# Optimization experiments

Hardware: AMD Instinct MI355X
Metric: run time of the kernel (lower is better)

## Reference

```python
import jax, jax.numpy as jnp
import numpy as np

N_NODES = 50000
N_EDGES = 600000
DIN, DH, DOUT = 128, 256, 128
BN_EPS = 1e-5
LRELU_SLOPE = 0.01


def setup_inputs() -> dict:
    key = jax.random.key(0)
    ks = jax.random.split(key, 16)
    rn = lambda k, s, sc=0.05: jax.random.normal(k, s, dtype=jnp.float32) * sc
    return {
        'nodes': jax.random.normal(ks[0], (N_NODES, DIN), dtype=jnp.float32),
        'src': jax.random.randint(ks[1], (N_EDGES,), 0, N_NODES, dtype=jnp.int32),
        'dst': jax.random.randint(ks[2], (N_EDGES,), 0, N_NODES, dtype=jnp.int32),
        # FeedForward params
        'Wf1': rn(ks[3], (DIN, DH)), 'bf1': jnp.zeros((DH,), jnp.float32),
        'gf1': jnp.ones((DH,), jnp.float32), 'bef1': jnp.zeros((DH,), jnp.float32),
        'Wf2': rn(ks[4], (DH, DIN)), 'bf2': jnp.zeros((DIN,), jnp.float32),
        'gf2': jnp.ones((DIN,), jnp.float32), 'bef2': jnp.zeros((DIN,), jnp.float32),
        # SAGEConv 1 (in->hidden)
        'Ws1': rn(ks[5], (DIN, DH)), 'Wn1': rn(ks[6], (DIN, DH)), 'b1': jnp.zeros((DH,), jnp.float32),
        'gs1': jnp.ones((DH,), jnp.float32), 'bs1': jnp.zeros((DH,), jnp.float32),
        # SAGEConv 2 (hidden->out)
        'Ws2': rn(ks[7], (DH, DOUT)), 'Wn2': rn(ks[8], (DH, DOUT)), 'b2': jnp.zeros((DOUT,), jnp.float32),
        'gs2': jnp.ones((DOUT,), jnp.float32), 'bs2': jnp.zeros((DOUT,), jnp.float32),
    }


def _bn(x, gamma, beta):
    # BatchNorm1d, training mode: batch stats over node dim, biased variance
    mu = jnp.mean(x, axis=0)
    var = jnp.mean(jnp.square(x - mu), axis=0)
    return (x - mu) * jax.lax.rsqrt(var + BN_EPS) * gamma + beta


def _sage_mean(x, src, dst, Wself, Wneigh, bias):
    # DGL SAGEConv('mean'): out = x@Wself + mean_{src->dst}(x[src])@Wneigh + bias
    n = x.shape[0]
    deg = jax.ops.segment_sum(jnp.ones_like(src, dtype=x.dtype), dst, num_segments=n)
    agg = jax.ops.segment_sum(x[src], dst, num_segments=n)  # [N, d] irregular scatter-add
    h_neigh = agg / jnp.maximum(deg, 1.0)[:, None]
    return x @ Wself + h_neigh @ Wneigh + bias


def reference(nodes, src, dst, Wf1, bf1, gf1, bef1, Wf2, bf2, gf2, bef2,
              Ws1, Wn1, b1, gs1, bs1, Ws2, Wn2, b2, gs2, bs2):
    # FeedForward (dropout=0 -> identity)
    h = jax.nn.relu(_bn(nodes @ Wf1 + bf1, gf1, bef1))
    h = jax.nn.relu(_bn(h @ Wf2 + bf2, gf2, bef2))
    # SAGE layer 1
    h1 = _sage_mean(h, src, dst, Ws1, Wn1, b1)
    h1 = jax.nn.leaky_relu(_bn(h1, gs1, bs1), LRELU_SLOPE)
    # SAGE layer 2
    h2 = _sage_mean(h1, src, dst, Ws2, Wn2, b2)
    return jax.nn.leaky_relu(_bn(h2, gs2, bs2), LRELU_SLOPE)
```

## Files before the change

kernel.cpp:

```cpp
#include <hip/hip_runtime.h>

#define DIN 128
#define BN_EPS 1e-5f

typedef __attribute__((ext_vector_type(8))) short bf16x8;
typedef __attribute__((ext_vector_type(8))) unsigned short us8;
typedef __attribute__((ext_vector_type(4))) float f32x4;

__device__ __forceinline__ ushort f2bf(float f) {
    unsigned u = __float_as_uint(f);
    u += 0x7fffu + ((u >> 16) & 1u);
    return (ushort)(u >> 16);
}
__device__ __forceinline__ float bf2f(ushort h) {
    return __uint_as_float(((unsigned)h) << 16);
}

template<int KC, int STATS>
__global__ __launch_bounds__(256) void gemm_wreg(
    const ushort* __restrict__ A, const ushort* __restrict__ BT,
    ushort* __restrict__ C, int mStrips, int N, int K, int logNG,
    float* __restrict__ gsums, float* __restrict__ gsqs)
{
    int tid = threadIdx.x;
    int lane = tid & 63;
    int gw = blockIdx.x * 4 + (tid >> 6);
    int wg = gw & ((1 << logNG) - 1);
    int set = gw >> logNG;
    int totalSets = (gridDim.x * 4) >> logNG;
    int cl = lane & 15, q = lane >> 4;
    int colBase = wg * 64;

    bf16x8 bf[4][KC];
    #pragma unroll
    for (int nt = 0; nt < 4; nt++) {
        const ushort* bp = BT + (long)(colBase + nt * 16 + cl) * K + q * 8;
        #pragma unroll
        for (int kc = 0; kc < KC; kc++)
            bf[nt][kc] = *(const bf16x8*)(bp + kc * 32);
    }

    float ssum[4] = {0.f, 0.f, 0.f, 0.f};
    float ssq[4]  = {0.f, 0.f, 0.f, 0.f};

    for (int strip = set; strip < mStrips; strip += totalSets) {
        int rowBase = strip * 16;
        const ushort* ap = A + (long)(rowBase + cl) * K + q * 8;
        bf16x8 af[KC];
        #pragma unroll
        for (int kc = 0; kc < KC; kc++)
            af[kc] = *(const bf16x8*)(ap + kc * 32);
        f32x4 acc[4] = {};
        #pragma unroll
        for (int kc = 0; kc < KC; kc++)
            #pragma unroll
            for (int nt = 0; nt < 4; nt++)
                acc[nt] = __builtin_amdgcn_mfma_f32_16x16x32_bf16(af[kc], bf[nt][kc], acc[nt], 0, 0, 0);
        #pragma unroll
        for (int nt = 0; nt < 4; nt++) {
            #pragma unroll
            for (int r = 0; r < 4; r++) {
                float v = acc[nt][r];
                long row = rowBase + q * 4 + r;
                C[row * N + colBase + nt * 16 + cl] = f2bf(v);
                if (STATS) { ssum[nt] += v; ssq[nt] += v * v; }
            }
        }
    }

    if (STATS) {
        #pragma unroll
        for (int nt = 0; nt < 4; nt++) {
            ssum[nt] += __shfl_xor(ssum[nt], 16, 64);
            ssum[nt] += __shfl_xor(ssum[nt], 32, 64);
            ssq[nt]  += __shfl_xor(ssq[nt], 16, 64);
            ssq[nt]  += __shfl_xor(ssq[nt], 32, 64);
        }
        if (q == 0) {
            #pragma unroll
            for (int nt = 0; nt < 4; nt++) {
                atomicAdd(&gsums[colBase + nt * 16 + cl], ssum[nt]);
                atomicAdd(&gsqs[colBase + nt * 16 + cl], ssq[nt]);
            }
        }
    }
}

__global__ __launch_bounds__(256) void setup_all(
    const float* __restrict__ nodes, ushort* __restrict__ Xbf, int nConv4, int nbConv,
    const float* __restrict__ W0, const float* __restrict__ W1,
    const float* __restrict__ W2, const float* __restrict__ W3,
    const float* __restrict__ W4, const float* __restrict__ W5,
    ushort* __restrict__ WT,
    int* __restrict__ zeroInts, int nZero4, int nbZero,
    float* __restrict__ stats)
{
    int b = blockIdx.x;
    int tid = threadIdx.x;
    if (b < nbConv) {
        int t = b * 256 + tid;
        if (t < nConv4) {
            float4 v = *(const float4*)&nodes[(long)t * 4];
            ushort4 o; o.x = f2bf(v.x); o.y = f2bf(v.y); o.z = f2bf(v.z); o.w = f2bf(v.w);
            *(ushort4*)&Xbf[(long)t * 4] = o;
        }
        return;
    }
    b -= nbConv;
    if (b < 768) {
        int seg = b >> 7;
        const float* W; int logK, dstBase, stride, kOff;
        switch (seg) {
            case 0: W = W0; logK = 7; dstBase = 0;      stride = 128; kOff = 0;   break;
            case 1: W = W1; logK = 8; dstBase = 32768;  stride = 256; kOff = 0;   break;
            case 2: W = W2; logK = 7; dstBase = 65536;  stride = 256; kOff = 0;   break;
            case 3: W = W3; logK = 7; dstBase = 65536;  stride = 256; kOff = 128; break;
            case 4: W = W4; logK = 8; dstBase = 131072; stride = 256; kOff = 0;   break;
            default:W = W5; logK = 8; dstBase = 163840; stride = 256; kOff = 0;   break;
        }
        int t = (b & 127) * 256 + tid;
        int N = 32768 >> logK;
        int k = t & ((1 << logK) - 1);
        int n = t >> logK;
        WT[(long)dstBase + (long)n * stride + kOff + k] = f2bf(W[(long)k * N + n]);
        return;
    }
    b -= 768;
    if (b < nbZero) {
        int t = b * 256 + tid;
        if (t < nZero4) *(int4*)&zeroInts[(long)t * 4] = make_int4(0, 0, 0, 0);
        return;
    }
    b -= nbZero;
    int t = b * 256 + tid;
    if (t < 512) *(float4*)&stats[(long)t * 4] = make_float4(0, 0, 0, 0);
}

template<int LOGN>
__global__ __launch_bounds__(256) void bnact_bf16(
    const ushort* __restrict__ X,
    const float* __restrict__ sums, const float* __restrict__ sqs,
    const float* __restrict__ gamma, const float* __restrict__ beta, float invM,
    ushort* __restrict__ O, int nRows, int outStride, float negSlope)
{
    constexpr int NCH = 1 << LOGN;
    __shared__ float ssc[NCH], ssh[NCH];
    int tid = threadIdx.x;
    if (tid < NCH) {
        float mean = sums[tid] * invM;
        float var = sqs[tid] * invM - mean * mean;
        float sc = gamma[tid] * rsqrtf(var + BN_EPS);
        ssc[tid] = sc;
        ssh[tid] = beta[tid] - mean * sc;
    }
    __syncthreads();
    int cb = (tid * 8) & (NCH - 1);
    float4 sA = *(const float4*)&ssc[cb];
    float4 sB = *(const float4*)&ssc[cb + 4];
    float4 hA = *(const float4*)&ssh[cb];
    float4 hB = *(const float4*)&ssh[cb + 4];
    const int rpb = (256 * 8) >> LOGN;
    int r0 = blockIdx.x * rpb + ((tid * 8) >> LOGN);
    int rstride = gridDim.x * rpb;
    for (int row = r0; row < nRows; row += rstride) {
        us8 v = *(const us8*)&X[(long)row * NCH + cb];
        float f0 = bf2f(v[0]) * sA.x + hA.x; f0 = (f0 > 0.f) ? f0 : f0 * negSlope;
        float f1 = bf2f(v[1]) * sA.y + hA.y; f1 = (f1 > 0.f) ? f1 : f1 * negSlope;
        float f2 = bf2f(v[2]) * sA.z + hA.z; f2 = (f2 > 0.f) ? f2 : f2 * negSlope;
        float f3 = bf2f(v[3]) * sA.w + hA.w; f3 = (f3 > 0.f) ? f3 : f3 * negSlope;
        float f4 = bf2f(v[4]) * sB.x + hB.x; f4 = (f4 > 0.f) ? f4 : f4 * negSlope;
        float f5 = bf2f(v[5]) * sB.y + hB.y; f5 = (f5 > 0.f) ? f5 : f5 * negSlope;
        float f6 = bf2f(v[6]) * sB.z + hB.z; f6 = (f6 > 0.f) ? f6 : f6 * negSlope;
        float f7 = bf2f(v[7]) * sB.w + hB.w; f7 = (f7 > 0.f) ? f7 : f7 * negSlope;
        us8 o;
        o[0] = f2bf(f0); o[1] = f2bf(f1); o[2] = f2bf(f2); o[3] = f2bf(f3);
        o[4] = f2bf(f4); o[5] = f2bf(f5); o[6] = f2bf(f6); o[7] = f2bf(f7);
        *(us8*)&O[(long)row * outStride + cb] = o;
    }
}

__global__ __launch_bounds__(256) void bnact_f32(
    float* __restrict__ X,
    const float* __restrict__ sums, const float* __restrict__ sqs,
    const float* __restrict__ gamma, const float* __restrict__ beta, float invM,
    int nRows, float negSlope)
{
    __shared__ float ssc[128], ssh[128];
    int tid = threadIdx.x;
    if (tid < 128) {
        float mean = sums[tid] * invM;
        float var = sqs[tid] * invM - mean * mean;
        float sc = gamma[tid] * rsqrtf(var + BN_EPS);
        ssc[tid] = sc;
        ssh[tid] = beta[tid] - mean * sc;
    }
    __syncthreads();
    int cb = (tid * 4) & 127;
    float4 sc = *(const float4*)&ssc[cb];
    float4 sh = *(const float4*)&ssh[cb];
    int r0 = blockIdx.x * 8 + ((tid * 4) >> 7);
    int rstride = gridDim.x * 8;
    for (int row = r0; row < nRows; row += rstride) {
        float4 v = *(const float4*)&X[(long)row * 128 + cb];
        float a = v.x * sc.x + sh.x; a = (a > 0.f) ? a : a * negSlope;
        float b = v.y * sc.y + sh.y; b = (b > 0.f) ? b : b * negSlope;
        float d = v.z * sc.z + sh.z; d = (d > 0.f) ? d : d * negSlope;
        float e = v.w * sc.w + sh.w; e = (e > 0.f) ? e : e * negSlope;
        *(float4*)&X[(long)row * 128 + cb] = make_float4(a, b, d, e);
    }
}

__global__ __launch_bounds__(256) void colstats128(
    const float* __restrict__ X, float* __restrict__ sums, float* __restrict__ sqs, int M)
{
    __shared__ float ss[128], sq[128];
    int tid = threadIdx.x;
    if (tid < 128) { ss[tid] = 0.f; sq[tid] = 0.f; }
    __syncthreads();
    int cg = tid & 31;
    int worker = (blockIdx.x << 3) | (tid >> 5);
    int totalW = gridDim.x << 3;
    float4 s4 = make_float4(0, 0, 0, 0), q4 = make_float4(0, 0, 0, 0);
    for (int r = worker; r < M; r += totalW) {
        float4 v = *(const float4*)&X[(long)r * 128 + cg * 4];
        s4.x += v.x; s4.y += v.y; s4.z += v.z; s4.w += v.w;
        q4.x += v.x * v.x; q4.y += v.y * v.y; q4.z += v.z * v.z; q4.w += v.w * v.w;
    }
    atomicAdd(&ss[cg * 4 + 0], s4.x); atomicAdd(&sq[cg * 4 + 0], q4.x);
    atomicAdd(&ss[cg * 4 + 1], s4.y); atomicAdd(&sq[cg * 4 + 1], q4.y);
    atomicAdd(&ss[cg * 4 + 2], s4.z); atomicAdd(&sq[cg * 4 + 2], q4.z);
    atomicAdd(&ss[cg * 4 + 3], s4.w); atomicAdd(&sq[cg * 4 + 3], q4.w);
    __syncthreads();
    if (tid < 128) { atomicAdd(&sums[tid], ss[tid]); atomicAdd(&sqs[tid], sq[tid]); }
}

__global__ void degcount_kernel(const int* __restrict__ dst, int* __restrict__ degi, int E)
{
    int i = blockIdx.x * blockDim.x + threadIdx.x;
    if (i < E) atomicAdd(&degi[dst[i]], 1);
}

__global__ __launch_bounds__(256) void scan_block_sums(const int* __restrict__ degi,
                                                       int* __restrict__ partial, int n)
{
    __shared__ int s[256];
    int i = blockIdx.x * 256 + threadIdx.x;
    s[threadIdx.x] = (i < n) ? degi[i] : 0;
    __syncthreads();
    for (int off = 128; off > 0; off >>= 1) {
        if (threadIdx.x < off) s[threadIdx.x] += s[threadIdx.x + off];
        __syncthreads();
    }
    if (threadIdx.x == 0) partial[blockIdx.x] = s[0];
}

__global__ __launch_bounds__(256) void scan_final(const int* __restrict__ degi,
                                                  const int* __restrict__ partial,
                                                  int* __restrict__ rowstart, int n, int nb)
{
    __shared__ int s[256];
    __shared__ int ps[256];
    int tid = threadIdx.x;
    ps[tid] = (tid < nb && tid < (int)blockIdx.x) ? partial[tid] : 0;
    __syncthreads();
    for (int off = 128; off > 0; off >>= 1) {
        if (tid < off) ps[tid] += ps[tid + off];
        __syncthreads();
    }
    int offset = ps[0];
    int i = blockIdx.x * 256 + tid;
    int v = (i < n) ? degi[i] : 0;
    s[tid] = v;
    __syncthreads();
    for (int off = 1; off < 256; off <<= 1) {
        int t = (tid >= off) ? s[tid - off] : 0;
        __syncthreads();
        s[tid] += t;
        __syncthreads();
    }
    if (i < n) rowstart[i] = offset + s[tid] - v;
}

__global__ void fillcsr_kernel(const int* __restrict__ src, const int* __restrict__ dst,
                               const int* __restrict__ rowstart, int* __restrict__ cursor,
                               int* __restrict__ csr, int E)
{
    int i = blockIdx.x * blockDim.x + threadIdx.x;
    if (i < E) {
        int d = dst[i];
        int p = atomicAdd(&cursor[d], 1);
        csr[rowstart[d] + p] = src[i];
    }
}

__device__ __forceinline__ void acc8(float acc[8], us8 v) {
    #pragma unroll
    for (int e = 0; e < 8; e++) acc[e] += bf2f(v[e]);
}

__global__ __launch_bounds__(256) void gather16_bf(
    const ushort* __restrict__ X, const int* __restrict__ rowstart,
    const int* __restrict__ degi, const int* __restrict__ csr,
    ushort* __restrict__ O, int nN)
{
    int wv = (blockIdx.x * blockDim.x + threadIdx.x) >> 6;
    int lane = threadIdx.x & 63;
    if (wv >= nN) return;
    int g = lane >> 4;
    int sc = lane & 15;
    int start = rowstart[wv], d = degi[wv];
    const ushort* Xc = X + sc * 8;
    float acc[8] = {};
    if (d > 0) {
        int dm = (d < 64) ? d : 64;
        int idx_l = csr[start + ((lane < dm) ? lane : (dm - 1))];
        int j = 0;
        for (; j + 8 <= dm; j += 8) {
            int i0 = __shfl(idx_l, j + g, 64);
            int i1 = __shfl(idx_l, j + 4 + g, 64);
            us8 v0 = *(const us8*)(Xc + (long)i0 * 256);
            us8 v1 = *(const us8*)(Xc + (long)i1 * 256);
            acc8(acc, v0);
            acc8(acc, v1);
        }
        if (j + 4 <= dm) {
            int i0 = __shfl(idx_l, j + g, 64);
            us8 v0 = *(const us8*)(Xc + (long)i0 * 256);
            acc8(acc, v0);
            j += 4;
        }
        int rem = dm - j;
        if (rem > 0) {
            int sl = j + ((g < rem) ? g : (rem - 1));
            int i0 = __shfl(idx_l, sl, 64);
            if (g < rem) {
                us8 v0 = *(const us8*)(Xc + (long)i0 * 256);
                acc8(acc, v0);
            }
        }
        for (int jj = 64; jj < d; jj += 4) {
            if (jj + g < d) {
                int i0 = csr[start + jj + g];
                us8 v0 = *(const us8*)(Xc + (long)i0 * 256);
                acc8(acc, v0);
            }
        }
    }
    #pragma unroll
    for (int e = 0; e < 8; e++) {
        acc[e] += __shfl_xor(acc[e], 16, 64);
        acc[e] += __shfl_xor(acc[e], 32, 64);
    }
    if (g == 0) {
        float inv = 1.f / fmaxf((float)d, 1.f);
        us8 o;
        #pragma unroll
        for (int e = 0; e < 8; e++) o[e] = f2bf(acc[e] * inv);
        *(us8*)(O + (long)wv * 256 + sc * 8) = o;
    }
}

__global__ __launch_bounds__(256) void gather16_fuse(
    const ushort* __restrict__ Z, const int* __restrict__ rowstart,
    const int* __restrict__ degi, const int* __restrict__ csr,
    float* __restrict__ O, int nN)
{
    int wv = (blockIdx.x * blockDim.x + threadIdx.x) >> 6;
    int lane = threadIdx.x & 63;
    if (wv >= nN) return;
    int g = lane >> 4;
    int sc = lane & 15;
    int start = rowstart[wv], d = degi[wv];
    const ushort* Zc = Z + sc * 8;
    us8 selfv = *(const us8*)(Zc + (long)wv * 256 + 128);
    float acc[8] = {};
    if (d > 0) {
        int dm = (d < 64) ? d : 64;
        int idx_l = csr[start + ((lane < dm) ? lane : (dm - 1))];
        int j = 0;
        for (; j + 8 <= dm; j += 8) {
            int i0 = __shfl(idx_l, j + g, 64);
            int i1 = __shfl(idx_l, j + 4 + g, 64);
            us8 v0 = *(const us8*)(Zc + (long)i0 * 256);
            us8 v1 = *(const us8*)(Zc + (long)i1 * 256);
            acc8(acc, v0);
            acc8(acc, v1);
        }
        if (j + 4 <= dm) {
            int i0 = __shfl(idx_l, j + g, 64);
            us8 v0 = *(const us8*)(Zc + (long)i0 * 256);
            acc8(acc, v0);
            j += 4;
        }
        int rem = dm - j;
        if (rem > 0) {
            int sl = j + ((g < rem) ? g : (rem - 1));
            int i0 = __shfl(idx_l, sl, 64);
            if (g < rem) {
                us8 v0 = *(const us8*)(Zc + (long)i0 * 256);
                acc8(acc, v0);
            }
        }
        for (int jj = 64; jj < d; jj += 4) {
            if (jj + g < d) {
                int i0 = csr[start + jj + g];
                us8 v0 = *(const us8*)(Zc + (long)i0 * 256);
                acc8(acc, v0);
            }
        }
    }
    #pragma unroll
    for (int e = 0; e < 8; e++) {
        acc[e] += __shfl_xor(acc[e], 16, 64);
        acc[e] += __shfl_xor(acc[e], 32, 64);
    }
    if (g == 0) {
        float inv = 1.f / fmaxf((float)d, 1.f);
        float r[8];
        #pragma unroll
        for (int e = 0; e < 8; e++) r[e] = acc[e] * inv + bf2f(selfv[e]);
        float* op = O + (long)wv * 128 + sc * 8;
        *(float4*)op = make_float4(r[0], r[1], r[2], r[3]);
        *(float4*)(op + 4) = make_float4(r[4], r[5], r[6], r[7]);
    }
}

extern "C" void kernel_launch(void* const* d_in, const int* in_sizes, int n_in,
                              void* d_out, int out_size, void* d_ws, size_t ws_size,
                              hipStream_t stream)
{
    const float* nodes = (const float*)d_in[0];
    const int*   src   = (const int*)d_in[1];
    const int*   dst   = (const int*)d_in[2];
    const float* Wf1   = (const float*)d_in[3];
    const float* gf1   = (const float*)d_in[5];
    const float* bef1  = (const float*)d_in[6];
    const float* Wf2   = (const float*)d_in[7];
    const float* gf2   = (const float*)d_in[9];
    const float* bef2  = (const float*)d_in[10];
    const float* Ws1   = (const float*)d_in[11];
    const float* Wn1   = (const float*)d_in[12];
    const float* gs1   = (const float*)d_in[14];
    const float* bs1   = (const float*)d_in[15];
    const float* Ws2   = (const float*)d_in[16];
    const float* Wn2   = (const float*)d_in[17];
    const float* gs2   = (const float*)d_in[19];
    const float* bs2   = (const float*)d_in[20];

    int nN = in_sizes[0] / DIN;
    int nE = in_sizes[1];
    float* out = (float*)d_out;
    int mStrips = nN / 16;
    float invM = 1.0f / nN;

    ushort* PRE = (ushort*)d_ws;
    ushort* BF1 = PRE + (size_t)nN * 256;
    ushort* BF2 = BF1 + (size_t)nN * 256;
    float* stats = (float*)(BF2 + (size_t)nN * 256);
    float* scale = stats + 2048;
    float* shift = scale + 256;
    ushort* WT   = (ushort*)(shift + 256);
    int* degi     = (int*)(WT + 196608);
    int* cursor   = degi + nN;
    int* rowstart = cursor + nN;
    int* partial  = rowstart + nN;
    int* csr      = partial + 256;

    ushort* Wf1T = WT;
    ushort* Wf2T = WT + 32768;
    ushort* Wc1T = WT + 65536;
    ushort* Wc2T = WT + 131072;

    dim3 blk(256);
    auto cdiv = [](int a, int b) { return (a + b - 1) / b; };
    int nScanBlocks = cdiv(nN, 256);

    int nConv4 = nN * DIN / 4;
    int nbConv = cdiv(nConv4, 256);
    int nZero4 = (2 * nN) / 4;
    int nbZero = cdiv(nZero4, 256);
    setup_all<<<dim3(nbConv + 768 + nbZero + 2), blk, 0, stream>>>(
        nodes, BF1, nConv4, nbConv,
        Wf1, Wf2, Ws1, Wn1, Wn2, Ws2, WT,
        degi, nZero4, nbZero, stats);

    degcount_kernel<<<dim3(cdiv(nE, 256)), blk, 0, stream>>>(dst, degi, nE);
    scan_block_sums<<<dim3(nScanBlocks), blk, 0, stream>>>(degi, partial, nN);
    scan_final<<<dim3(nScanBlocks), blk, 0, stream>>>(degi, partial, rowstart, nN, nScanBlocks);
    fillcsr_kernel<<<dim3(cdiv(nE, 256)), blk, 0, stream>>>(src, dst, rowstart, cursor, csr, nE);

    gemm_wreg<4, 1><<<dim3(512), blk, 0, stream>>>(BF1, Wf1T, PRE, mStrips, 256, 128, 2, stats, stats + 256);
    bnact_bf16<8><<<dim3(2048), blk, 0, stream>>>(PRE, stats, stats + 256, gf1, bef1, invM,
                                                  BF1, nN, 256, 0.0f);

    gemm_wreg<8, 1><<<dim3(256), blk, 0, stream>>>(BF1, Wf2T, PRE, mStrips, 128, 256, 1, stats + 512, stats + 768);
    bnact_bf16<7><<<dim3(2048), blk, 0, stream>>>(PRE, stats + 512, stats + 768, gf2, bef2, invM,
                                                  BF2, nN, 256, 0.0f);

    gather16_bf<<<dim3(cdiv(nN * 64, 256)), blk, 0, stream>>>(BF2, rowstart, degi, csr, BF2 + 128, nN);

    gemm_wreg<8, 1><<<dim3(512), blk, 0, stream>>>(BF2, Wc1T, PRE, mStrips, 256, 256, 2, stats + 1024, stats + 1280);
    bnact_bf16<8><<<dim3(2048), blk, 0, stream>>>(PRE, stats + 1024, stats + 1280, gs1, bs1, invM,
                                                  BF1, nN, 256, 0.01f);

    gemm_wreg<8, 0><<<dim3(512), blk, 0, stream>>>(BF1, Wc2T, BF2, mStrips, 256, 256, 2, nullptr, nullptr);
    gather16_fuse<<<dim3(cdiv(nN * 64, 256)), blk, 0, stream>>>(BF2, rowstart, degi, csr, out, nN);

    colstats128<<<dim3(120), blk, 0, stream>>>(out, stats + 1536, stats + 1792, nN);
    bnact_f32<<<dim3(2048), blk, 0, stream>>>(out, stats + 1536, stats + 1792, gs2, bs2, invM,
                                              nN, 0.01f);
}
```

Measured before the change: 392.3 us.

## Transpose MFMA output for vectorized GEMM stores and unroll gathers branch-free

The GEMM swaps the MFMA operand order so each lane holds four consecutive output columns of one row. This allows a single 8-byte vector store per tile instead of four scattered 2-byte stores. BN statistics are now kept per column element and reduced across the 16 row lanes before the atomics. The neighbor gathers are restructured to issue four independent row loads per iteration, with masked weights replacing the tail branches to raise memory-level parallelism, at the cost of redundant loads for padded slots.

Result: slower. 509.6 us (+29.9%).

```diff
diff --git a/kernel.cpp b/kernel.cpp
--- a/kernel.cpp
+++ b/kernel.cpp
@@ -40,8 +40,8 @@
             bf[nt][kc] = *(const bf16x8*)(bp + kc * 32);
     }
 
-    float ssum[4] = {0.f, 0.f, 0.f, 0.f};
-    float ssq[4]  = {0.f, 0.f, 0.f, 0.f};
+    float ssum[4][4] = {};
+    float ssq[4][4]  = {};
 
     for (int strip = set; strip < mStrips; strip += totalSets) {
         int rowBase = strip * 16;
@@ -55,32 +55,43 @@
         for (int kc = 0; kc < KC; kc++)
             #pragma unroll
             for (int nt = 0; nt < 4; nt++)
-                acc[nt] = __builtin_amdgcn_mfma_f32_16x16x32_bf16(af[kc], bf[nt][kc], acc[nt], 0, 0, 0);
+                acc[nt] = __builtin_amdgcn_mfma_f32_16x16x32_bf16(bf[nt][kc], af[kc], acc[nt], 0, 0, 0);
+        long row = rowBase + cl;
         #pragma unroll
         for (int nt = 0; nt < 4; nt++) {
+            ushort4 o;
+            float v0 = acc[nt][0], v1 = acc[nt][1], v2 = acc[nt][2], v3 = acc[nt][3];
+            o.x = f2bf(v0); o.y = f2bf(v1); o.z = f2bf(v2); o.w = f2bf(v3);
+            *(ushort4*)&C[row * N + colBase + nt * 16 + q * 4] = o;
+            if (STATS) {
+                ssum[nt][0] += v0; ssq[nt][0] += v0 * v0;
+                ssum[nt][1] += v1; ssq[nt][1] += v1 * v1;
+                ssum[nt][2] += v2; ssq[nt][2] += v2 * v2;
+                ssum[nt][3] += v3; ssq[nt][3] += v3 * v3;
+            }
+        }
+    }
+
+    if (STATS) {
+        #pragma unroll
+        for (int nt = 0; nt < 4; nt++) {
             #pragma unroll
             for (int r = 0; r < 4; r++) {
-                float v = acc[nt][r];
-                long row = rowBase + q * 4 + r;
-                C[row * N + colBase + nt * 16 + cl] = f2bf(v);
-                if (STATS) { ssum[nt] += v; ssq[nt] += v * v; }
-            }
-        }
-    }
-
-    if (STATS) {
-        #pragma unroll
-        for (int nt = 0; nt < 4; nt++) {
-            ssum[nt] += __shfl_xor(ssum[nt], 16, 64);
-            ssum[nt] += __shfl_xor(ssum[nt], 32, 64);
-            ssq[nt]  += __shfl_xor(ssq[nt], 16, 64);
-            ssq[nt]  += __shfl_xor(ssq[nt], 32, 64);
-        }
-        if (q == 0) {
+                #pragma unroll
+                for (int m = 1; m < 16; m <<= 1) {
+                    ssum[nt][r] += __shfl_xor(ssum[nt][r], m, 64);
+                    ssq[nt][r]  += __shfl_xor(ssq[nt][r], m, 64);
+                }
+            }
+        }
+        if (cl == 0) {
             #pragma unroll
             for (int nt = 0; nt < 4; nt++) {
-                atomicAdd(&gsums[colBase + nt * 16 + cl], ssum[nt]);
-                atomicAdd(&gsqs[colBase + nt * 16 + cl], ssq[nt]);
+                #pragma unroll
+                for (int r = 0; r < 4; r++) {
+                    atomicAdd(&gsums[colBase + nt * 16 + q * 4 + r], ssum[nt][r]);
+                    atomicAdd(&gsqs[colBase + nt * 16 + q * 4 + r], ssq[nt][r]);
+                }
             }
         }
     }
@@ -293,11 +304,6 @@
     }
 }
 
-__device__ __forceinline__ void acc8(float acc[8], us8 v) {
-    #pragma unroll
-    for (int e = 0; e < 8; e++) acc[e] += bf2f(v[e]);
-}
-
 __global__ __launch_bounds__(256) void gather16_bf(
     const ushort* __restrict__ X, const int* __restrict__ rowstart,
     const int* __restrict__ degi, const int* __restrict__ csr,
@@ -314,35 +320,28 @@
     if (d > 0) {
         int dm = (d < 64) ? d : 64;
         int idx_l = csr[start + ((lane < dm) ? lane : (dm - 1))];
-        int j = 0;
-        for (; j + 8 <= dm; j += 8) {
-            int i0 = __shfl(idx_l, j + g, 64);
-            int i1 = __shfl(idx_l, j + 4 + g, 64);
-            us8 v0 = *(const us8*)(Xc + (long)i0 * 256);
-            us8 v1 = *(const us8*)(Xc + (long)i1 * 256);
-            acc8(acc, v0);
-            acc8(acc, v1);
-        }
-        if (j + 4 <= dm) {
-            int i0 = __shfl(idx_l, j + g, 64);
-            us8 v0 = *(const us8*)(Xc + (long)i0 * 256);
-            acc8(acc, v0);
-            j += 4;
-        }
-        int rem = dm - j;
-        if (rem > 0) {
-            int sl = j + ((g < rem) ? g : (rem - 1));
-            int i0 = __shfl(idx_l, sl, 64);
-            if (g < rem) {
-                us8 v0 = *(const us8*)(Xc + (long)i0 * 256);
-                acc8(acc, v0);
-            }
+        for (int j = 0; j < dm; j += 16) {
+            us8 v[4]; float w[4];
+            #pragma unroll
+            for (int b = 0; b < 4; b++) {
+                int slot = j + b * 4 + g;
+                int cs = (slot < dm) ? slot : (dm - 1);
+                int idx = __shfl(idx_l, cs, 64);
+                v[b] = *(const us8*)(Xc + (long)idx * 256);
+                w[b] = (slot < dm) ? 1.f : 0.f;
+            }
+            #pragma unroll
+            for (int b = 0; b < 4; b++)
+                #pragma unroll
+                for (int e = 0; e < 8; e++)
+                    acc[e] += w[b] * bf2f(v[b][e]);
         }
         for (int jj = 64; jj < d; jj += 4) {
             if (jj + g < d) {
                 int i0 = csr[start + jj + g];
                 us8 v0 = *(const us8*)(Xc + (long)i0 * 256);
-                acc8(acc, v0);
+                #pragma unroll
+                for (int e = 0; e < 8; e++) acc[e] += bf2f(v0[e]);
             }
         }
     }
@@ -377,35 +376,28 @@
     if (d > 0) {
         int dm = (d < 64) ? d : 64;
         int idx_l = csr[start + ((lane < dm) ? lane : (dm - 1))];
-        int j = 0;
-        for (; j + 8 <= dm; j += 8) {
-            int i0 = __shfl(idx_l, j + g, 64);
-            int i1 = __shfl(idx_l, j + 4 + g, 64);
-            us8 v0 = *(const us8*)(Zc + (long)i0 * 256);
-            us8 v1 = *(const us8*)(Zc + (long)i1 * 256);
-            acc8(acc, v0);
-            acc8(acc, v1);
-        }
-        if (j + 4 <= dm) {
-            int i0 = __shfl(idx_l, j + g, 64);
-            us8 v0 = *(const us8*)(Zc + (long)i0 * 256);
-            acc8(acc, v0);
-            j += 4;
-        }
-        int rem = dm - j;
-        if (rem > 0) {
-            int sl = j + ((g < rem) ? g : (rem - 1));
-            int i0 = __shfl(idx_l, sl, 64);
-            if (g < rem) {
-                us8 v0 = *(const us8*)(Zc + (long)i0 * 256);
-                acc8(acc, v0);
-            }
+        for (int j = 0; j < dm; j += 16) {
+            us8 v[4]; float w[4];
+            #pragma unroll
+            for (int b = 0; b < 4; b++) {
+                int slot = j + b * 4 + g;
+                int cs = (slot < dm) ? slot : (dm - 1);
+                int idx = __shfl(idx_l, cs, 64);
+                v[b] = *(const us8*)(Zc + (long)idx * 256);
+                w[b] = (slot < dm) ? 1.f : 0.f;
+            }
+            #pragma unroll
+            for (int b = 0; b < 4; b++)
+                #pragma unroll
+                for (int e = 0; e < 8; e++)
+                    acc[e] += w[b] * bf2f(v[b][e]);
         }
         for (int jj = 64; jj < d; jj += 4) {
             if (jj + g < d) {
                 int i0 = csr[start + jj + g];
                 us8 v0 = *(const us8*)(Zc + (long)i0 * 256);
-                acc8(acc, v0);
+                #pragma unroll
+                for (int e = 0; e < 8; e++) acc[e] += bf2f(v0[e]);
             }
         }
     }
```
